# Kernel optimization log

Measured on AMD Instinct MI355X. Metric: run time of the kernel, lower is better.

The kernel has to match this reference:

```python
import jax, jax.numpy as jnp
import numpy as np

N = 8192          # num_nodes
FEAT = 512        # pca_dim + neighbor_dim
C = 40            # num_classes
HID = 1024
OUT = 40
HOPS = 4


def setup_inputs() -> dict:
    key = jax.random.key(0)
    k_x, k_adj, k_lab, k_w1, k_w2 = jax.random.split(key, 5)
    X = jax.random.normal(k_x, (N, FEAT), dtype=jnp.float32)
    # one-hot labels, as the module expects
    labels = jax.random.randint(k_lab, (N,), 0, C)
    onehot_labels = jax.nn.one_hot(labels, C, dtype=jnp.float32)
    adj_logits = jax.random.normal(k_adj, (N, N), dtype=jnp.float32)
    in_dim = FEAT + HOPS * C  # 672, must match Linear(input_dim, hidden_dim)
    W1 = jax.random.normal(k_w1, (in_dim, HID), dtype=jnp.float32) * (1.0 / np.sqrt(in_dim))
    b1 = jnp.zeros((HID,), dtype=jnp.float32)
    W2 = jax.random.normal(k_w2, (HID, OUT), dtype=jnp.float32) * (1.0 / np.sqrt(HID))
    b2 = jnp.zeros((OUT,), dtype=jnp.float32)
    return {"X": X, "onehot_labels": onehot_labels, "adj_logits": adj_logits,
            "W1": W1, "b1": b1, "W2": W2, "b2": b2, "max_hops": HOPS}


def reference(X, onehot_labels, adj_logits, W1, b1, W2, b2, max_hops):
    A_hat = jax.nn.sigmoid(adj_logits)                     # [N, N]
    # D_inv @ A_hat is just row scaling; avoid materializing diag(N,N)
    d_inv = 1.0 / (A_hat.sum(axis=1) + 1e-8)               # [N]
    A_norm = A_hat * d_inv[:, None]                        # [N, N]
    cur = onehot_labels                                    # [N, C]
    dists = []
    for _ in range(max_hops):                              # small fixed hop count
        cur = jax.nn.softmax(A_norm @ cur, axis=1)         # [N, C]
        dists.append(cur)
    combined = jnp.concatenate([X] + dists, axis=1)        # [N, FEAT + hops*C]
    h = jax.nn.relu(combined @ W1 + b1)                    # [N, HID]
    return h @ W2 + b2                                     # [N, OUT]
```

## Files before the change

kernel.cpp:

```cpp
#include <hip/hip_runtime.h>
#include <hip/hip_bf16.h>

#define NN 8192
#define CFEAT 512
#define NCLS 40
#define NPAD 48
#define INDIM 672
#define HIDD 1024

typedef __attribute__((ext_vector_type(8))) short bf16x8;
typedef __attribute__((ext_vector_type(4))) float f32x4;

#define A_SCALE 1048576.0f
#define A_INV_SCALE 9.5367431640625e-07f

__device__ inline unsigned short f2b(float f) {
  union { __hip_bfloat16 b; unsigned short u; } cv;
  cv.b = __float2bfloat16(f);
  return cv.u;
}

__device__ inline unsigned char f2fp8(float f) {
  int pk = __builtin_amdgcn_cvt_pk_fp8_f32(f, 0.f, 0, false);
  return (unsigned char)(pk & 0xff);
}

__device__ inline size_t ilv_off(int r, int G) {
  return (size_t)(r >> 4) * 131072 + (size_t)(G >> 7) * 16384 +
         (size_t)((G >> 2) & 31) * 512 + (size_t)(G & 3) * 128 + (size_t)(r & 15) * 8;
}

__global__ __launch_bounds__(256) void normalize_kernel(const float* __restrict__ adj,
                                                        unsigned char* __restrict__ A8) {
  __shared__ float wsum[4];
  const int t = threadIdx.x;
  const size_t i = blockIdx.x;
  const float4* src = (const float4*)(adj + i * NN);
  float4 v[8];
  float sum = 0.f;
#pragma unroll
  for (int it = 0; it < 8; ++it) {
    float4 x = src[it * 256 + t];
    float s0 = __builtin_amdgcn_rcpf(1.f + __expf(-x.x));
    float s1 = __builtin_amdgcn_rcpf(1.f + __expf(-x.y));
    float s2 = __builtin_amdgcn_rcpf(1.f + __expf(-x.z));
    float s3 = __builtin_amdgcn_rcpf(1.f + __expf(-x.w));
    v[it] = make_float4(s0, s1, s2, s3);
    sum += (s0 + s1) + (s2 + s3);
  }
#pragma unroll
  for (int m = 1; m < 64; m <<= 1) sum += __shfl_xor(sum, m);
  if ((t & 63) == 0) wsum[t >> 6] = sum;
  __syncthreads();
  const float dinv = A_SCALE / (wsum[0] + wsum[1] + wsum[2] + wsum[3] + 1e-8f);
  unsigned char* base = A8 + (size_t)(i >> 4) * 131072 + (size_t)(t >> 3) * 512 +
                        (size_t)((t >> 1) & 3) * 128 + (size_t)(i & 15) * 8 + (size_t)(t & 1) * 4;
#pragma unroll
  for (int it = 0; it < 8; ++it) {
    int lo = __builtin_amdgcn_cvt_pk_fp8_f32(v[it].x * dinv, v[it].y * dinv, 0, false);
    int pk = __builtin_amdgcn_cvt_pk_fp8_f32(v[it].z * dinv, v[it].w * dinv, lo, true);
    *(unsigned int*)(base + (size_t)it * 16384) = (unsigned int)pk;
  }
}

__global__ __launch_bounds__(256) void prep_kernel(const float* __restrict__ X,
                                                   const float* __restrict__ onehot,
                                                   const float* __restrict__ W1,
                                                   const float* __restrict__ W2,
                                                   unsigned short* __restrict__ comb,
                                                   unsigned char* __restrict__ curT0,
                                                   unsigned short* __restrict__ W1T,
                                                   unsigned short* __restrict__ W2T) {
  const int NX = NN * CFEAT;
  const int NO = NCLS * NN;
  const int NW1 = INDIM * HIDD;
  const int NW2 = HIDD * NCLS;
  const int total = NX + NO + NW1 + NW2;
  for (int idx = blockIdx.x * 256 + threadIdx.x; idx < total; idx += gridDim.x * 256) {
    if (idx < NX) {
      int i = idx >> 9, c = idx & 511;
      comb[(size_t)i * INDIM + c] = f2b(X[idx]);
    } else if (idx < NX + NO) {
      int t = idx - NX;
      int c = t >> 13, i = t & 8191;
      curT0[ilv_off(c, i >> 3) + (i & 7)] = f2fp8(onehot[(size_t)i * NCLS + c]);
    } else if (idx < NX + NO + NW1) {
      int t = idx - NX - NO;
      int k = t >> 10, n = t & 1023;
      W1T[(size_t)n * INDIM + k] = f2b(W1[t]);
    } else {
      int t = idx - NX - NO - NW1;
      int k = t / NCLS, c = t - k * NCLS;
      W2T[(size_t)c * HIDD + k] = f2b(W2[t]);
    }
  }
}

__global__ __launch_bounds__(512) void hop_kernel(const unsigned char* __restrict__ A8,
                                                  const unsigned char* __restrict__ curT,
                                                  unsigned char* __restrict__ nextT,
                                                  unsigned short* __restrict__ comb,
                                                  int hop) {
  __shared__ float red[8][16][NPAD];
  const int lane = threadIdx.x & 63;
  const int wave = threadIdx.x >> 6;
  const int l15 = lane & 15;
  const int kg = lane >> 4;
  const long* ap  = (const long*)(A8  + (size_t)blockIdx.x * 131072 + (size_t)wave * 16384) + lane;
  const long* bp0 = (const long*)(curT +                              (size_t)wave * 16384) + lane;
  const long* bp1 = (const long*)(curT + 131072                     + (size_t)wave * 16384) + lane;
  const long* bp2 = (const long*)(curT + 262144                     + (size_t)wave * 16384) + lane;
  f32x4 acc0 = {0.f, 0.f, 0.f, 0.f}, acc1 = {0.f, 0.f, 0.f, 0.f}, acc2 = {0.f, 0.f, 0.f, 0.f};
#pragma unroll 4
  for (int t = 0; t < 32; ++t) {
    long a  = ap[t * 64];
    long b0 = bp0[t * 64];
    long b1 = bp1[t * 64];
    long b2 = bp2[t * 64];
    acc0 = __builtin_amdgcn_mfma_f32_16x16x32_fp8_fp8(a, b0, acc0, 0, 0, 0);
    acc1 = __builtin_amdgcn_mfma_f32_16x16x32_fp8_fp8(a, b1, acc1, 0, 0, 0);
    acc2 = __builtin_amdgcn_mfma_f32_16x16x32_fp8_fp8(a, b2, acc2, 0, 0, 0);
  }
#pragma unroll
  for (int r = 0; r < 4; ++r) {
    red[wave][kg * 4 + r][l15] = acc0[r];
    red[wave][kg * 4 + r][16 + l15] = acc1[r];
    red[wave][kg * 4 + r][32 + l15] = acc2[r];
  }
  __syncthreads();
  if (wave < 4) {
    const int rr = kg * 4 + wave;
    float v0 = 0.f, v1 = 0.f, v2 = 0.f;
#pragma unroll
    for (int w = 0; w < 8; ++w) {
      v0 += red[w][rr][l15];
      v1 += red[w][rr][16 + l15];
      v2 += red[w][rr][32 + l15];
    }
    v0 *= A_INV_SCALE; v1 *= A_INV_SCALE; v2 *= A_INV_SCALE;
    const bool ok2 = l15 < 8;
    float m = fmaxf(v0, v1);
    if (ok2) m = fmaxf(m, v2);
#pragma unroll
    for (int s = 1; s < 16; s <<= 1) m = fmaxf(m, __shfl_xor(m, s));
    float e0 = __expf(v0 - m);
    float e1 = __expf(v1 - m);
    float e2 = ok2 ? __expf(v2 - m) : 0.f;
    float ssum = e0 + e1 + e2;
#pragma unroll
    for (int s = 1; s < 16; s <<= 1) ssum += __shfl_xor(ssum, s);
    const float inv = 1.f / ssum;
    const size_t i = (size_t)blockIdx.x * 16 + rr;
    const float p0 = e0 * inv;
    const float p1 = e1 * inv;
    const int G = (int)(i >> 3);
    const size_t joff = (size_t)(G >> 7) * 16384 + (size_t)((G >> 2) & 31) * 512 +
                        (size_t)(G & 3) * 128 + (i & 7);
    nextT[joff + (size_t)l15 * 8] = f2fp8(p0);
    nextT[131072 + joff + (size_t)l15 * 8] = f2fp8(p1);
    const size_t cbase = i * INDIM + CFEAT + (size_t)hop * NCLS;
    comb[cbase + l15] = f2b(p0);
    comb[cbase + 16 + l15] = f2b(p1);
    if (ok2) {
      const float p2 = e2 * inv;
      nextT[262144 + joff + (size_t)l15 * 8] = f2fp8(p2);
      comb[cbase + 32 + l15] = f2b(p2);
    }
  }
}

__global__ __launch_bounds__(256) void gemm1_kernel(const unsigned short* __restrict__ comb,
                                                    const unsigned short* __restrict__ W1T,
                                                    const float* __restrict__ bias1,
                                                    unsigned short* __restrict__ h) {
  const int lane = threadIdx.x & 63;
  const int wave = threadIdx.x >> 6;
  const int l15 = lane & 15;
  const int kg = lane >> 4;
  const int bm = blockIdx.x & 127;
  const int bn = blockIdx.x >> 7;
  const size_t arow = (size_t)bm * 64 + wave * 16 + l15;
  const bf16x8* ap = (const bf16x8*)(comb + arow * INDIM + (size_t)kg * 8);
  const bf16x8* bp[8];
#pragma unroll
  for (int tt = 0; tt < 8; ++tt)
    bp[tt] = (const bf16x8*)(W1T + (size_t)(bn * 128 + tt * 16 + l15) * INDIM + (size_t)kg * 8);
  f32x4 acc[8] = {};
#pragma unroll 3
  for (int kk = 0; kk < INDIM; kk += 32) {
    bf16x8 a = *ap; ap += 4;
#pragma unroll
    for (int tt = 0; tt < 8; ++tt) {
      bf16x8 b = *bp[tt]; bp[tt] += 4;
      acc[tt] = __builtin_amdgcn_mfma_f32_16x16x32_bf16(a, b, acc[tt], 0, 0, 0);
    }
  }
#pragma unroll
  for (int tt = 0; tt < 8; ++tt) {
    const int n = bn * 128 + tt * 16 + l15;
    const float bv = bias1[n];
#pragma unroll
    for (int r = 0; r < 4; ++r) {
      const size_t i = (size_t)bm * 64 + wave * 16 + kg * 4 + r;
      float v = acc[tt][r] + bv;
      h[i * HIDD + n] = f2b(v > 0.f ? v : 0.f);
    }
  }
}

__global__ __launch_bounds__(256) void gemm2_kernel(const unsigned short* __restrict__ h,
                                                    const unsigned short* __restrict__ W2T,
                                                    const float* __restrict__ bias2,
                                                    float* __restrict__ out) {
  __shared__ float red[4][16][NPAD];
  const int lane = threadIdx.x & 63;
  const int wave = threadIdx.x >> 6;
  const int l15 = lane & 15;
  const int kg = lane >> 4;
  const size_t arow = (size_t)blockIdx.x * 16 + l15;
  const size_t kbase = (size_t)wave * 256 + (size_t)kg * 8;
  const bf16x8* ap = (const bf16x8*)(h + arow * HIDD + kbase);
  const bf16x8* bp0 = (const bf16x8*)(W2T + (size_t)l15 * HIDD + kbase);
  const bf16x8* bp1 = (const bf16x8*)(W2T + (size_t)(16 + l15) * HIDD + kbase);
  const bf16x8* bp2 = (const bf16x8*)(W2T + (size_t)(32 + l15) * HIDD + kbase);
  f32x4 acc0 = {0.f, 0.f, 0.f, 0.f}, acc1 = {0.f, 0.f, 0.f, 0.f}, acc2 = {0.f, 0.f, 0.f, 0.f};
#pragma unroll
  for (int kk = 0; kk < 256; kk += 32) {
    bf16x8 a = *ap; ap += 4;
    bf16x8 vb0 = *bp0; bp0 += 4;
    bf16x8 vb1 = *bp1; bp1 += 4;
    bf16x8 vb2 = *bp2; bp2 += 4;
    acc0 = __builtin_amdgcn_mfma_f32_16x16x32_bf16(a, vb0, acc0, 0, 0, 0);
    acc1 = __builtin_amdgcn_mfma_f32_16x16x32_bf16(a, vb1, acc1, 0, 0, 0);
    acc2 = __builtin_amdgcn_mfma_f32_16x16x32_bf16(a, vb2, acc2, 0, 0, 0);
  }
#pragma unroll
  for (int r = 0; r < 4; ++r) {
    red[wave][kg * 4 + r][l15] = acc0[r];
    red[wave][kg * 4 + r][16 + l15] = acc1[r];
    red[wave][kg * 4 + r][32 + l15] = acc2[r];
  }
  __syncthreads();
  if (wave == 0) {
#pragma unroll
    for (int r = 0; r < 4; ++r) {
      const int rr = kg * 4 + r;
      float v0 = red[0][rr][l15] + red[1][rr][l15] + red[2][rr][l15] + red[3][rr][l15];
      float v1 = red[0][rr][16 + l15] + red[1][rr][16 + l15] + red[2][rr][16 + l15] + red[3][rr][16 + l15];
      float v2 = red[0][rr][32 + l15] + red[1][rr][32 + l15] + red[2][rr][32 + l15] + red[3][rr][32 + l15];
      const size_t i = (size_t)blockIdx.x * 16 + rr;
      out[i * NCLS + l15] = v0 + bias2[l15];
      out[i * NCLS + 16 + l15] = v1 + bias2[16 + l15];
      if (l15 < 8) out[i * NCLS + 32 + l15] = v2 + bias2[32 + l15];
    }
  }
}

extern "C" void kernel_launch(void* const* d_in, const int* in_sizes, int n_in,
                              void* d_out, int out_size, void* d_ws, size_t ws_size,
                              hipStream_t stream) {
  const float* X = (const float*)d_in[0];
  const float* onehot = (const float*)d_in[1];
  const float* adj = (const float*)d_in[2];
  const float* W1 = (const float*)d_in[3];
  const float* b1 = (const float*)d_in[4];
  const float* W2 = (const float*)d_in[5];
  const float* b2 = (const float*)d_in[6];
  float* out = (float*)d_out;
  char* ws = (char*)d_ws;

  unsigned char*  A8   = (unsigned char*)(ws);
  unsigned char*  cur0 = (unsigned char*)(ws + 67108864ull);
  unsigned char*  cur1 = (unsigned char*)(ws + 67502080ull);
  unsigned short* comb = (unsigned short*)(ws + 67895296ull);
  unsigned short* W1T  = (unsigned short*)(ws + 78905344ull);
  unsigned short* W2T  = (unsigned short*)(ws + 80281600ull);
  unsigned short* hbuf = (unsigned short*)(ws + 80379904ull);

  normalize_kernel<<<NN, 256, 0, stream>>>(adj, A8);
  prep_kernel<<<2048, 256, 0, stream>>>(X, onehot, W1, W2, comb, cur0, W1T, W2T);
  hop_kernel<<<NN / 16, 512, 0, stream>>>(A8, cur0, cur1, comb, 0);
  hop_kernel<<<NN / 16, 512, 0, stream>>>(A8, cur1, cur0, comb, 1);
  hop_kernel<<<NN / 16, 512, 0, stream>>>(A8, cur0, cur1, comb, 2);
  hop_kernel<<<NN / 16, 512, 0, stream>>>(A8, cur1, cur0, comb, 3);
  gemm1_kernel<<<1024, 256, 0, stream>>>(comb, W1T, b1, hbuf);
  gemm2_kernel<<<NN / 16, 256, 0, stream>>>(hbuf, W2T, b2, out);
}
```

Before: 602.4 us.

## Defer row normalization to hop kernel and coalesce interleaved A8 writes via LDS

The sigmoid kernel now quantizes sigmoid values with a fixed scale instead of the per-row normalized value, and stores 1/(scale*rowsum) separately so the hop kernel applies it after the matmul. Each block handles 16 rows and stages their fp8 values in LDS, then writes the interleaved MFMA layout as contiguous 16-byte chunks instead of scattered 4-byte stores. This targets uncoalesced writes in the bandwidth-bound 256MB read pass. It adds LDS traffic and block syncs, and changes fp8 quantization precision, since sigmoid values now sit in a fixed range rather than being scaled by 2^20/rowsum.

New measurement: 539.6 us. 10.4% less time.

```diff
diff --git a/kernel.cpp b/kernel.cpp
--- a/kernel.cpp
+++ b/kernel.cpp
@@ -10,9 +10,9 @@
 
 typedef __attribute__((ext_vector_type(8))) short bf16x8;
 typedef __attribute__((ext_vector_type(4))) float f32x4;
-
-#define A_SCALE 1048576.0f
-#define A_INV_SCALE 9.5367431640625e-07f
+typedef __attribute__((ext_vector_type(2))) long l64x2;
+
+#define SIG_SCALE 32.0f
 
 __device__ inline unsigned short f2b(float f) {
   union { __hip_bfloat16 b; unsigned short u; } cv;
@@ -30,37 +30,47 @@
          (size_t)((G >> 2) & 31) * 512 + (size_t)(G & 3) * 128 + (size_t)(r & 15) * 8;
 }
 
-__global__ __launch_bounds__(256) void normalize_kernel(const float* __restrict__ adj,
-                                                        unsigned char* __restrict__ A8) {
-  __shared__ float wsum[4];
+__global__ __launch_bounds__(1024) void sig_kernel(const float* __restrict__ adj,
+                                                   unsigned char* __restrict__ A8i,
+                                                   float* __restrict__ dinv) {
+  __shared__ unsigned char lds[16][2056];
   const int t = threadIdx.x;
-  const size_t i = blockIdx.x;
-  const float4* src = (const float4*)(adj + i * NN);
-  float4 v[8];
+  const int wave = t >> 6;
+  const int lane = t & 63;
+  const size_t grp = blockIdx.x;
+  const size_t row = grp * 16 + wave;
+  const float4* src = (const float4*)(adj + row * NN);
+  unsigned char* dst = A8i + grp * 131072;
   float sum = 0.f;
-#pragma unroll
-  for (int it = 0; it < 8; ++it) {
-    float4 x = src[it * 256 + t];
-    float s0 = __builtin_amdgcn_rcpf(1.f + __expf(-x.x));
-    float s1 = __builtin_amdgcn_rcpf(1.f + __expf(-x.y));
-    float s2 = __builtin_amdgcn_rcpf(1.f + __expf(-x.z));
-    float s3 = __builtin_amdgcn_rcpf(1.f + __expf(-x.w));
-    v[it] = make_float4(s0, s1, s2, s3);
-    sum += (s0 + s1) + (s2 + s3);
-  }
-#pragma unroll
-  for (int m = 1; m < 64; m <<= 1) sum += __shfl_xor(sum, m);
-  if ((t & 63) == 0) wsum[t >> 6] = sum;
-  __syncthreads();
-  const float dinv = A_SCALE / (wsum[0] + wsum[1] + wsum[2] + wsum[3] + 1e-8f);
-  unsigned char* base = A8 + (size_t)(i >> 4) * 131072 + (size_t)(t >> 3) * 512 +
-                        (size_t)((t >> 1) & 3) * 128 + (size_t)(i & 15) * 8 + (size_t)(t & 1) * 4;
-#pragma unroll
-  for (int it = 0; it < 8; ++it) {
-    int lo = __builtin_amdgcn_cvt_pk_fp8_f32(v[it].x * dinv, v[it].y * dinv, 0, false);
-    int pk = __builtin_amdgcn_cvt_pk_fp8_f32(v[it].z * dinv, v[it].w * dinv, lo, true);
-    *(unsigned int*)(base + (size_t)it * 16384) = (unsigned int)pk;
-  }
+  for (int m = 0; m < 4; ++m) {
+#pragma unroll
+    for (int it = 0; it < 8; ++it) {
+      const int idx = it * 64 + lane;
+      float4 x = src[m * 512 + idx];
+      float s0 = __builtin_amdgcn_rcpf(1.f + __expf(-x.x));
+      float s1 = __builtin_amdgcn_rcpf(1.f + __expf(-x.y));
+      float s2 = __builtin_amdgcn_rcpf(1.f + __expf(-x.z));
+      float s3 = __builtin_amdgcn_rcpf(1.f + __expf(-x.w));
+      sum += (s0 + s1) + (s2 + s3);
+      int lo = __builtin_amdgcn_cvt_pk_fp8_f32(s0 * SIG_SCALE, s1 * SIG_SCALE, 0, false);
+      int pk = __builtin_amdgcn_cvt_pk_fp8_f32(s2 * SIG_SCALE, s3 * SIG_SCALE, lo, true);
+      *(unsigned int*)&lds[wave][idx * 4] = (unsigned int)pk;
+    }
+    __syncthreads();
+#pragma unroll
+    for (int pass = 0; pass < 2; ++pass) {
+      const int v = pass * 1024 + t;
+      const int g = v >> 3, q = v & 7;
+      l64x2 val;
+      val[0] = *(const long*)&lds[2 * q][g * 8];
+      val[1] = *(const long*)&lds[2 * q + 1][g * 8];
+      *(l64x2*)(dst + (size_t)m * 32768 + (size_t)v * 16) = val;
+    }
+    __syncthreads();
+  }
+#pragma unroll
+  for (int s = 1; s < 64; s <<= 1) sum += __shfl_xor(sum, s);
+  if (lane == 0) dinv[row] = 1.f / (SIG_SCALE * (sum + 1e-8f));
 }
 
 __global__ __launch_bounds__(256) void prep_kernel(const float* __restrict__ X,
@@ -98,6 +108,7 @@
 
 __global__ __launch_bounds__(512) void hop_kernel(const unsigned char* __restrict__ A8,
                                                   const unsigned char* __restrict__ curT,
+                                                  const float* __restrict__ dinv,
                                                   unsigned char* __restrict__ nextT,
                                                   unsigned short* __restrict__ comb,
                                                   int hop) {
@@ -130,6 +141,8 @@
   __syncthreads();
   if (wave < 4) {
     const int rr = kg * 4 + wave;
+    const size_t i = (size_t)blockIdx.x * 16 + rr;
+    const float dv = dinv[i];
     float v0 = 0.f, v1 = 0.f, v2 = 0.f;
 #pragma unroll
     for (int w = 0; w < 8; ++w) {
@@ -137,7 +150,7 @@
       v1 += red[w][rr][16 + l15];
       v2 += red[w][rr][32 + l15];
     }
-    v0 *= A_INV_SCALE; v1 *= A_INV_SCALE; v2 *= A_INV_SCALE;
+    v0 *= dv; v1 *= dv; v2 *= dv;
     const bool ok2 = l15 < 8;
     float m = fmaxf(v0, v1);
     if (ok2) m = fmaxf(m, v2);
@@ -150,7 +163,6 @@
 #pragma unroll
     for (int s = 1; s < 16; s <<= 1) ssum += __shfl_xor(ssum, s);
     const float inv = 1.f / ssum;
-    const size_t i = (size_t)blockIdx.x * 16 + rr;
     const float p0 = e0 * inv;
     const float p1 = e1 * inv;
     const int G = (int)(i >> 3);
@@ -269,20 +281,21 @@
   float* out = (float*)d_out;
   char* ws = (char*)d_ws;
 
-  unsigned char*  A8   = (unsigned char*)(ws);
-  unsigned char*  cur0 = (unsigned char*)(ws + 67108864ull);
-  unsigned char*  cur1 = (unsigned char*)(ws + 67502080ull);
-  unsigned short* comb = (unsigned short*)(ws + 67895296ull);
-  unsigned short* W1T  = (unsigned short*)(ws + 78905344ull);
-  unsigned short* W2T  = (unsigned short*)(ws + 80281600ull);
-  unsigned short* hbuf = (unsigned short*)(ws + 80379904ull);
-
-  normalize_kernel<<<NN, 256, 0, stream>>>(adj, A8);
+  unsigned char*  A8i  = (unsigned char*)(ws);
+  float*          dinv = (float*)(ws + 67108864ull);
+  unsigned char*  cur0 = (unsigned char*)(ws + 67141632ull);
+  unsigned char*  cur1 = (unsigned char*)(ws + 67534848ull);
+  unsigned short* comb = (unsigned short*)(ws + 67928064ull);
+  unsigned short* W1T  = (unsigned short*)(ws + 78938112ull);
+  unsigned short* W2T  = (unsigned short*)(ws + 80314368ull);
+  unsigned short* hbuf = (unsigned short*)(ws + 80412672ull);
+
+  sig_kernel<<<NN / 16, 1024, 0, stream>>>(adj, A8i, dinv);
   prep_kernel<<<2048, 256, 0, stream>>>(X, onehot, W1, W2, comb, cur0, W1T, W2T);
-  hop_kernel<<<NN / 16, 512, 0, stream>>>(A8, cur0, cur1, comb, 0);
-  hop_kernel<<<NN / 16, 512, 0, stream>>>(A8, cur1, cur0, comb, 1);
-  hop_kernel<<<NN / 16, 512, 0, stream>>>(A8, cur0, cur1, comb, 2);
-  hop_kernel<<<NN / 16, 512, 0, stream>>>(A8, cur1, cur0, comb, 3);
+  hop_kernel<<<NN / 16, 512, 0, stream>>>(A8i, cur0, dinv, cur1, comb, 0);
+  hop_kernel<<<NN / 16, 512, 0, stream>>>(A8i, cur1, dinv, cur0, comb, 1);
+  hop_kernel<<<NN / 16, 512, 0, stream>>>(A8i, cur0, dinv, cur1, comb, 2);
+  hop_kernel<<<NN / 16, 512, 0, stream>>>(A8i, cur1, dinv, cur0, comb, 3);
   gemm1_kernel<<<1024, 256, 0, stream>>>(comb, W1T, b1, hbuf);
   gemm2_kernel<<<NN / 16, 256, 0, stream>>>(hbuf, W2T, b2, out);
 }
```
